# Optimization experiments

Measured on AMD Instinct MI355X. Metric: run time of the kernel, lower is better.

Reference implementation:

```python
import jax, jax.numpy as jnp
import numpy as np

D = 768
B = 32
N = 768


def setup_inputs() -> dict:
    key = jax.random.key(0)
    k1, k2, k3, k4 = jax.random.split(key, 4)
    stdv = 1.0 / np.sqrt(D)
    X = jax.random.normal(k1, (B, N, D), dtype=jnp.float32)
    adj = jax.random.uniform(k2, (B, N, N), dtype=jnp.float32)
    W_l = jax.random.uniform(k3, (D, D), dtype=jnp.float32, minval=-stdv, maxval=stdv)
    W_l1 = jax.random.uniform(k4, (D, D), dtype=jnp.float32, minval=-stdv, maxval=stdv)
    return {"X": X, "adj": adj, "W_l": W_l, "W_l1": W_l1}


def _row_normalize(adj):
    # rowsum^-1 with inf -> 0 (rows summing to zero stay zero)
    rowsum = adj.sum(axis=-1, keepdims=True)  # [B, N, 1]
    r_inv = jnp.where(rowsum == 0, 0.0, 1.0 / rowsum)
    return adj * r_inv


def reference(X, adj, W_l, W_l1):
    # X: [B, N, D], adj: [B, N, N]
    adj_n = _row_normalize(adj)
    e1 = jnp.einsum('bnd,de->bne', X, W_l1)        # message transform
    e11 = jnp.einsum('bnm,bmd->bnd', adj_n, e1)    # aggregate
    X1 = jnp.einsum('bnd,de->bne', X, W_l)         # self transform
    h = X1 + e11
    return jax.nn.leaky_relu(h, negative_slope=0.01)
```

## Files before the change

### kernel.cpp

```cpp
#include <hip/hip_runtime.h>
#include <hip/hip_bf16.h>
#include <cstdint>
#include <cstddef>

#define BN_ROWS 24576
#define DD 768
#define BE (768*768)
#define BM 192
#define BN_T 192
#define BK 32
#define ABUF 12288
#define BUFSZ 24576

typedef __attribute__((ext_vector_type(8))) short bf16x8;
typedef __attribute__((ext_vector_type(4))) float f32x4;
typedef __attribute__((ext_vector_type(8))) unsigned short u16x8;

static __device__ __forceinline__ unsigned short f2bf(float f) {
  unsigned int u = __builtin_bit_cast(unsigned int, f);
  unsigned int lsb = (u >> 16) & 1u;
  u += 0x7fffu + lsb;
  return (unsigned short)(u >> 16);
}

static __device__ __forceinline__ unsigned short f2bfv(float f) {
  __hip_bfloat16 h = __float2bfloat16(f);
  return __builtin_bit_cast(unsigned short, h);
}

static __device__ __forceinline__ bf16x8 cvt8(float4 u, float4 w, float sc) {
  bf16x8 o;
  o[0] = (short)f2bfv(u.x * sc); o[1] = (short)f2bfv(u.y * sc);
  o[2] = (short)f2bfv(u.z * sc); o[3] = (short)f2bfv(u.w * sc);
  o[4] = (short)f2bfv(w.x * sc); o[5] = (short)f2bfv(w.y * sc);
  o[6] = (short)f2bfv(w.z * sc); o[7] = (short)f2bfv(w.w * sc);
  return o;
}


#define P_AN 3072
#define P_WT 144
#define P_FL 288

__global__ __launch_bounds__(256) void prep(const float* __restrict__ adj,
                                            const float* __restrict__ Wl,
                                            const float* __restrict__ Wl1,
                                            unsigned short* __restrict__ adjnb,
                                            unsigned short* __restrict__ WlT,
                                            unsigned short* __restrict__ Wl1T) {
  __shared__ float tile[64][65];
  const int bid = blockIdx.x;
  if (bid < P_AN) {
    const int w = threadIdx.x >> 6;
    const int hl = (threadIdx.x >> 5) & 1;
    const int l = threadIdx.x & 31;
    const int row = bid * 8 + w * 2 + hl;
    const float4* a = reinterpret_cast<const float4*>(adj + (size_t)row * DD);
    float4 v[6];
    #pragma unroll
    for (int i = 0; i < 3; ++i) {
      int u = l + i * 32;
      v[2 * i]     = a[u * 2];
      v[2 * i + 1] = a[u * 2 + 1];
    }
    float s = 0.f;
    #pragma unroll
    for (int i = 0; i < 6; ++i) s += (v[i].x + v[i].y) + (v[i].z + v[i].w);
    #pragma unroll
    for (int off = 16; off; off >>= 1) s += __shfl_xor(s, off);
    float rinv = (s == 0.f) ? 0.f : 1.f / s;
    u16x8* o = reinterpret_cast<u16x8*>(adjnb + (size_t)row * DD);
    #pragma unroll
    for (int i = 0; i < 3; ++i)
      o[l + i * 32] = __builtin_bit_cast(u16x8, cvt8(v[2 * i], v[2 * i + 1], rinv));
  } else if (bid < P_AN + P_WT) {
    const int tb = bid - P_AN;
    const int tr = tb / 12, tc = tb % 12;
    const int c = threadIdx.x & 63, r0 = threadIdx.x >> 6;
    #pragma unroll
    for (int i = 0; i < 16; ++i) {
      int r = r0 + i * 4;
      tile[r][c] = Wl1[(size_t)(tr * 64 + r) * DD + tc * 64 + c];
    }
    __syncthreads();
    #pragma unroll
    for (int i = 0; i < 16; ++i) {
      int r2 = r0 + i * 4;
      Wl1T[(size_t)(tc * 64 + r2) * DD + tr * 64 + c] = f2bf(tile[c][r2]);
    }
  } else {
    const int b2 = bid - (P_AN + P_WT);
    const int wg = b2 * 4 + (threadIdx.x >> 6);
    const int lane = threadIdx.x & 63;
    const int d0 = (wg % 96) * 8;
    const int e = (wg / 96) * 64 + lane;
    u16x8 o;
    #pragma unroll
    for (int j = 0; j < 8; ++j)
      o[j] = f2bf(Wl[(size_t)(d0 + j) * DD + e]);
    const int base = ((e >> 4) * 24 + (d0 >> 5)) * 512
                   + ((e & 15) + (((d0 >> 3) & 3) << 4)) * 8;
    *reinterpret_cast<u16x8*>(WlT + base) = o;
  }
}

__global__ __launch_bounds__(256, 2) void gemm_e1(
    const float* __restrict__ X,
    const unsigned short* __restrict__ W1T,
    unsigned short* __restrict__ e1T,
    unsigned short* __restrict__ Xb)
{
  __shared__ char smem[2 * BUFSZ];
  constexpr int NT = 24;
  const int tid = threadIdx.x, lane = tid & 63;
  const int wid = tid >> 6;
  const int wr = wid >> 1, wc = wid & 1;

  const int logical = (blockIdx.x & 7) * 64 + (blockIdx.x >> 3);
  const int mt = logical >> 2, nt = logical & 3;
  const int b = mt >> 2;
  const float* Ag = X + (size_t)mt * BM * DD;
  const unsigned short* Bg = W1T + (size_t)nt * BN_T * DD;

  const int r_in = lane >> 2;
  const int s_in = lane & 3;

  float4 aR[3][2];
  auto issueA = [&](int s) {
    int kk = s < NT ? s : 0;
    #pragma unroll
    for (int i = 0; i < 3; ++i) {
      int row = (wid * 3 + i) * 16 + r_in;
      int slot = s_in ^ ((row >> 1) & 3);
      const float4* p = reinterpret_cast<const float4*>(
          Ag + (size_t)row * DD + kk * BK + slot * 8);
      aR[i][0] = p[0];
      aR[i][1] = p[1];
    }
  };
  auto writeA = [&](int s) {
    const int buf = (s & 1) * BUFSZ;
    #pragma unroll
    for (int i = 0; i < 3; ++i)
      *reinterpret_cast<bf16x8*>(smem + buf + (wid * 3 + i) * 1024 + lane * 16) =
          cvt8(aR[i][0], aR[i][1], 1.0f);
  };
  auto storeXb = [&](int s) {
    int kk = s < NT ? s : 0;
    #pragma unroll
    for (int i = 0; i < 3; ++i) {
      int row = (wid * 3 + i) * 16 + r_in;
      int slot = s_in ^ ((row >> 1) & 3);
      *reinterpret_cast<bf16x8*>(Xb + (size_t)(mt * BM + row) * DD + kk * BK + slot * 8) =
          cvt8(aR[i][0], aR[i][1], 1.0f);
    }
  };
  auto issueB = [&](int s) {
    int kk = s < NT ? s : 0;
    const int buf = (s & 1) * BUFSZ + ABUF;
    #pragma unroll
    for (int i = 0; i < 3; ++i) {
      int c = wid * 3 + i;
      int row = c * 16 + r_in;
      int slot = s_in ^ ((row >> 1) & 3);
      const unsigned short* src = Bg + (size_t)row * DD + kk * BK + slot * 8;
      __builtin_amdgcn_global_load_lds(
          (const __attribute__((address_space(1))) void*)src,
          (__attribute__((address_space(3))) void*)(smem + buf + c * 1024),
          16, 0, 0);
    }
  };

  const int ks = lane >> 4;
  auto frag = [&](int off, int row) -> bf16x8 {
    int slot = ks ^ ((row >> 1) & 3);
    return *reinterpret_cast<const bf16x8*>(smem + off + row * 64 + slot * 16);
  };

  f32x4 acc[6][6] = {};
  const int arow = wr * 96 + (lane & 15);
  const int brow = wc * 96 + (lane & 15);

  issueA(0);
  asm volatile("s_waitcnt vmcnt(0)" ::: "memory");
  writeA(0);
  issueB(0);
  issueA(1);
  asm volatile("s_waitcnt lgkmcnt(0)" ::: "memory");
  __builtin_amdgcn_s_barrier();

  for (int t = 0; t < NT; ++t) {
    asm volatile("s_waitcnt vmcnt(6)" ::: "memory");
    __builtin_amdgcn_s_barrier();
    issueB(t + 1);

    const int bufA = (t & 1) * BUFSZ;
    const int bufB = bufA + ABUF;
    bf16x8 a[6], bg[6];
    #pragma unroll
    for (int i = 0; i < 6; ++i) a[i] = frag(bufA, arow + i * 16);
    #pragma unroll
    for (int i = 0; i < 6; ++i) bg[i] = frag(bufB, brow + i * 16);

    __builtin_amdgcn_s_setprio(1);
    #pragma unroll
    for (int ni = 0; ni < 6; ++ni)
      #pragma unroll
      for (int mi = 0; mi < 6; ++mi)
        acc[mi][ni] = __builtin_amdgcn_mfma_f32_16x16x32_bf16(a[mi], bg[ni], acc[mi][ni], 0, 0, 0);
    __builtin_amdgcn_s_setprio(0);

    asm volatile("s_waitcnt vmcnt(3)" ::: "memory");
    writeA(t + 1);
    if (nt == 0) storeXb(t + 1);
    issueA(t + 2);
    asm volatile("s_waitcnt lgkmcnt(0)" ::: "memory");
  }

  unsigned short* ob = e1T + (size_t)b * BE;
  const int m0 = (mt & 3) * BM + wr * 96 + (lane >> 4) * 4;
  const int l15 = lane & 15;
  #pragma unroll
  for (int mi = 0; mi < 6; ++mi)
    #pragma unroll
    for (int ni = 0; ni < 6; ++ni) {
      int m = m0 + mi * 16;
      int cb = nt * 12 + wc * 6 + ni;
      int fa = (cb * 24 + (m >> 5)) * 512
             + (l15 + (((m >> 3) & 3) << 4)) * 8 + (m & 7);
      f32x4 v = acc[mi][ni];
      ushort4 o;
      o.x = f2bf(v[0]); o.y = f2bf(v[1]); o.z = f2bf(v[2]); o.w = f2bf(v[3]);
      *reinterpret_cast<ushort4*>(ob + fa) = o;
    }
}

__global__ __launch_bounds__(256, 2) void gemm_bg(
    const unsigned short* __restrict__ adjnb,
    const unsigned short* __restrict__ e1T,
    const unsigned short* __restrict__ Xb,
    const unsigned short* __restrict__ WlT,
    float* __restrict__ out)
{
  __shared__ char smem[24576];
  constexpr int NT = 48;
  const int tid = threadIdx.x, lane = tid & 63;
  const int wid = tid >> 6;
  const int wr = wid >> 1, wc = wid & 1;

  const int logical = (blockIdx.x & 7) * 64 + (blockIdx.x >> 3);
  const int b = logical >> 4;
  const int r = logical & 15;
  const int mt = r >> 2, nt = r & 3;
  const size_t bo = (size_t)b * BE;
  const unsigned short* A0 = adjnb + bo + (size_t)mt * BM * DD;
  const unsigned short* A1 = Xb + bo + (size_t)mt * BM * DD;
  const unsigned short* B0 = e1T + bo;
  const unsigned short* B1 = WlT;

  const int r_in = lane >> 2;
  const int s_in = lane & 3;
  const int colblk0 = nt * 12 + wc * 6;

  auto stage = [&](int s) {
    int sc = s < NT ? s : 0;
    const unsigned short* base = (sc >= 24) ? A1 : A0;
    int kk = (sc >= 24) ? sc - 24 : sc;
    const int buf = (s & 1) * 12288;
    #pragma unroll
    for (int i = 0; i < 3; ++i) {
      int chunk = wid * 3 + i;
      int row = chunk * 16 + r_in;
      int slot = s_in ^ ((row >> 1) & 3);
      const unsigned short* src = base + (size_t)row * DD + kk * BK + slot * 8;
      __builtin_amdgcn_global_load_lds(
          (const __attribute__((address_space(1))) void*)src,
          (__attribute__((address_space(3))) void*)(smem + buf + chunk * 1024),
          16, 0, 0);
    }
  };

  auto loadB = [&](int s, bf16x8* dst) {
    int sc = s < NT ? s : 0;
    const unsigned short* base = (sc >= 24) ? B1 : B0;
    int kk = (sc >= 24) ? sc - 24 : sc;
    #pragma unroll
    for (int ni = 0; ni < 6; ++ni)
      dst[ni] = *reinterpret_cast<const bf16x8*>(
          base + ((colblk0 + ni) * 24 + kk) * 512 + lane * 8);
  };

  const int ks = lane >> 4;
  auto rdA = [&](int off, int row) -> bf16x8 {
    int slot = ks ^ ((row >> 1) & 3);
    return *reinterpret_cast<const bf16x8*>(smem + off + row * 64 + slot * 16);
  };

  f32x4 acc[6][6] = {};
  const int arow = wr * 96 + (lane & 15);
  bf16x8 bA[6], bB[6];

  auto body = [&](int bufo, bf16x8* bfr) {
    #pragma unroll
    for (int mh = 0; mh < 2; ++mh) {
      bf16x8 a[3];
      #pragma unroll
      for (int i = 0; i < 3; ++i) a[i] = rdA(bufo, arow + mh * 48 + i * 16);
      __builtin_amdgcn_s_setprio(1);
      #pragma unroll
      for (int mi = 0; mi < 3; ++mi)
        #pragma unroll
        for (int ni = 0; ni < 6; ++ni)
          acc[mh * 3 + mi][ni] = __builtin_amdgcn_mfma_f32_16x16x32_bf16(
              a[mi], bfr[ni], acc[mh * 3 + mi][ni], 0, 0, 0);
      __builtin_amdgcn_s_setprio(0);
    }
  };

  stage(0); loadB(0, bA);
  for (int t = 0; t < NT; t += 2) {
    asm volatile("s_waitcnt vmcnt(6)" ::: "memory");
    __builtin_amdgcn_s_barrier();
    stage(t + 1); loadB(t + 1, bB);
    body(0, bA);
    asm volatile("s_waitcnt vmcnt(6)" ::: "memory");
    __builtin_amdgcn_s_barrier();
    stage(t + 2); loadB(t + 2, bA);
    body(12288, bB);
  }
  asm volatile("s_waitcnt vmcnt(0)" ::: "memory");

  float* ob = out + bo;
  const int m0 = mt * BM + wr * 96 + (lane >> 4) * 4;
  const int l15 = lane & 15;
  #pragma unroll
  for (int mi = 0; mi < 6; ++mi)
    #pragma unroll
    for (int ni = 0; ni < 6; ++ni) {
      int m = m0 + mi * 16;
      int n = nt * BN_T + wc * 96 + ni * 16 + l15;
      f32x4 v = acc[mi][ni];
      #pragma unroll
      for (int j = 0; j < 4; ++j) {
        float x = v[j];
        ob[(size_t)(m + j) * DD + n] = x > 0.f ? x : 0.01f * x;
      }
    }
}


extern "C" void kernel_launch(void* const* d_in, const int* in_sizes, int n_in,
                              void* d_out, int out_size, void* d_ws, size_t ws_size,
                              hipStream_t stream) {
  const float* X   = (const float*)d_in[0];
  const float* adj = (const float*)d_in[1];
  const float* Wl  = (const float*)d_in[2];
  const float* Wl1 = (const float*)d_in[3];
  float* out = (float*)d_out;

  char* ws = (char*)d_ws;
  const size_t SZ = (size_t)BN_ROWS * DD * 2;
  unsigned short* e1T   = (unsigned short*)(ws);
  unsigned short* adjnb = (unsigned short*)(ws + SZ);
  unsigned short* Xb    = (unsigned short*)(ws + 2 * SZ);
  unsigned short* WlT   = (unsigned short*)(ws + 3 * SZ);
  unsigned short* Wl1T  = (unsigned short*)(ws + 3 * SZ + (size_t)BE * 2);

  prep<<<P_AN + P_WT + P_FL, 256, 0, stream>>>(adj, Wl, Wl1, adjnb, WlT, Wl1T);
  gemm_e1<<<512, 256, 0, stream>>>(X, Wl1T, e1T, Xb);
  gemm_bg<<<512, 256, 0, stream>>>(adjnb, e1T, Xb, WlT, out);
}
```

Baseline: 157.9 us.

## Compute X·W_l in first GEMM kernel and add it in the aggregate epilogue

After: 154.1 us. 2.4% less time.

```diff
diff --git a/kernel.cpp b/kernel.cpp
--- a/kernel.cpp
+++ b/kernel.cpp
@@ -7,10 +7,7 @@
 #define DD 768
 #define BE (768*768)
 #define BM 192
-#define BN_T 192
 #define BK 32
-#define ABUF 12288
-#define BUFSZ 24576
 
 typedef __attribute__((ext_vector_type(8))) short bf16x8;
 typedef __attribute__((ext_vector_type(4))) float f32x4;
@@ -22,24 +19,29 @@
   u += 0x7fffu + lsb;
   return (unsigned short)(u >> 16);
 }
-
 static __device__ __forceinline__ unsigned short f2bfv(float f) {
   __hip_bfloat16 h = __float2bfloat16(f);
   return __builtin_bit_cast(unsigned short, h);
 }
-
-static __device__ __forceinline__ bf16x8 cvt8(float4 u, float4 w, float sc) {
+static __device__ __forceinline__ bf16x8 cvt8(float4 u, float4 w) {
   bf16x8 o;
-  o[0] = (short)f2bfv(u.x * sc); o[1] = (short)f2bfv(u.y * sc);
-  o[2] = (short)f2bfv(u.z * sc); o[3] = (short)f2bfv(u.w * sc);
-  o[4] = (short)f2bfv(w.x * sc); o[5] = (short)f2bfv(w.y * sc);
-  o[6] = (short)f2bfv(w.z * sc); o[7] = (short)f2bfv(w.w * sc);
+  o[0] = (short)f2bfv(u.x); o[1] = (short)f2bfv(u.y);
+  o[2] = (short)f2bfv(u.z); o[3] = (short)f2bfv(u.w);
+  o[4] = (short)f2bfv(w.x); o[5] = (short)f2bfv(w.y);
+  o[6] = (short)f2bfv(w.z); o[7] = (short)f2bfv(w.w);
   return o;
 }
+static __device__ __forceinline__ u16x8 pack8s(float4 a, float4 b, float sc) {
+  u16x8 o;
+  o[0] = f2bfv(a.x * sc); o[1] = f2bfv(a.y * sc);
+  o[2] = f2bfv(a.z * sc); o[3] = f2bfv(a.w * sc);
+  o[4] = f2bfv(b.x * sc); o[5] = f2bfv(b.y * sc);
+  o[6] = f2bfv(b.z * sc); o[7] = f2bfv(b.w * sc);
+  return o;
+}
 
 
 #define P_AN 3072
-#define P_WT 144
 #define P_FL 288
 
 __global__ __launch_bounds__(256) void prep(const float* __restrict__ adj,
@@ -48,7 +50,6 @@
                                             unsigned short* __restrict__ adjnb,
                                             unsigned short* __restrict__ WlT,
                                             unsigned short* __restrict__ Wl1T) {
-  __shared__ float tile[64][65];
   const int bid = blockIdx.x;
   if (bid < P_AN) {
     const int w = threadIdx.x >> 6;
@@ -72,55 +73,46 @@
     u16x8* o = reinterpret_cast<u16x8*>(adjnb + (size_t)row * DD);
     #pragma unroll
     for (int i = 0; i < 3; ++i)
-      o[l + i * 32] = __builtin_bit_cast(u16x8, cvt8(v[2 * i], v[2 * i + 1], rinv));
-  } else if (bid < P_AN + P_WT) {
-    const int tb = bid - P_AN;
-    const int tr = tb / 12, tc = tb % 12;
-    const int c = threadIdx.x & 63, r0 = threadIdx.x >> 6;
-    #pragma unroll
-    for (int i = 0; i < 16; ++i) {
-      int r = r0 + i * 4;
-      tile[r][c] = Wl1[(size_t)(tr * 64 + r) * DD + tc * 64 + c];
-    }
-    __syncthreads();
-    #pragma unroll
-    for (int i = 0; i < 16; ++i) {
-      int r2 = r0 + i * 4;
-      Wl1T[(size_t)(tc * 64 + r2) * DD + tr * 64 + c] = f2bf(tile[c][r2]);
-    }
+      o[l + i * 32] = pack8s(v[2 * i], v[2 * i + 1], rinv);
   } else {
-    const int b2 = bid - (P_AN + P_WT);
-    const int wg = b2 * 4 + (threadIdx.x >> 6);
+    const int b2 = bid - P_AN;
+    const bool isWl = b2 < P_FL;
+    const int b3 = isWl ? b2 : b2 - P_FL;
+    const float* src = isWl ? Wl : Wl1;
+    unsigned short* dst = isWl ? WlT : Wl1T;
+    const int wg = b3 * 4 + (threadIdx.x >> 6);
     const int lane = threadIdx.x & 63;
     const int d0 = (wg % 96) * 8;
     const int e = (wg / 96) * 64 + lane;
     u16x8 o;
     #pragma unroll
     for (int j = 0; j < 8; ++j)
-      o[j] = f2bf(Wl[(size_t)(d0 + j) * DD + e]);
+      o[j] = f2bf(src[(size_t)(d0 + j) * DD + e]);
     const int base = ((e >> 4) * 24 + (d0 >> 5)) * 512
                    + ((e & 15) + (((d0 >> 3) & 3) << 4)) * 8;
-    *reinterpret_cast<u16x8*>(WlT + base) = o;
+    *reinterpret_cast<u16x8*>(dst + base) = o;
   }
 }
 
-__global__ __launch_bounds__(256, 2) void gemm_e1(
+__global__ __launch_bounds__(256, 2) void e1w(
     const float* __restrict__ X,
-    const unsigned short* __restrict__ W1T,
+    const unsigned short* __restrict__ Wl1T,
+    const unsigned short* __restrict__ WlT,
     unsigned short* __restrict__ e1T,
-    unsigned short* __restrict__ Xb)
+    unsigned short* __restrict__ X1f)
 {
-  __shared__ char smem[2 * BUFSZ];
+  __shared__ char smem[2 * 12288];
   constexpr int NT = 24;
   const int tid = threadIdx.x, lane = tid & 63;
   const int wid = tid >> 6;
   const int wr = wid >> 1, wc = wid & 1;
 
-  const int logical = (blockIdx.x & 7) * 64 + (blockIdx.x >> 3);
-  const int mt = logical >> 2, nt = logical & 3;
+  const int logical = (blockIdx.x & 7) * 128 + (blockIdx.x >> 3);
+  const int mt = logical >> 3, nt = logical & 7;
   const int b = mt >> 2;
   const float* Ag = X + (size_t)mt * BM * DD;
-  const unsigned short* Bg = W1T + (size_t)nt * BN_T * DD;
+  const unsigned short* Bfl = (nt < 4) ? Wl1T : WlT;
+  const int colblk0 = (nt & 3) * 12 + wc * 6;
 
   const int r_in = lane >> 2;
   const int s_in = lane & 3;
@@ -139,111 +131,114 @@
     }
   };
   auto writeA = [&](int s) {
-    const int buf = (s & 1) * BUFSZ;
+    const int buf = (s & 1) * 12288;
     #pragma unroll
     for (int i = 0; i < 3; ++i)
       *reinterpret_cast<bf16x8*>(smem + buf + (wid * 3 + i) * 1024 + lane * 16) =
-          cvt8(aR[i][0], aR[i][1], 1.0f);
-  };
-  auto storeXb = [&](int s) {
+          cvt8(aR[i][0], aR[i][1]);
+  };
+  auto loadB = [&](int s, bf16x8* dst) {
     int kk = s < NT ? s : 0;
     #pragma unroll
-    for (int i = 0; i < 3; ++i) {
-      int row = (wid * 3 + i) * 16 + r_in;
-      int slot = s_in ^ ((row >> 1) & 3);
-      *reinterpret_cast<bf16x8*>(Xb + (size_t)(mt * BM + row) * DD + kk * BK + slot * 8) =
-          cvt8(aR[i][0], aR[i][1], 1.0f);
-    }
-  };
-  auto issueB = [&](int s) {
-    int kk = s < NT ? s : 0;
-    const int buf = (s & 1) * BUFSZ + ABUF;
-    #pragma unroll
-    for (int i = 0; i < 3; ++i) {
-      int c = wid * 3 + i;
-      int row = c * 16 + r_in;
-      int slot = s_in ^ ((row >> 1) & 3);
-      const unsigned short* src = Bg + (size_t)row * DD + kk * BK + slot * 8;
-      __builtin_amdgcn_global_load_lds(
-          (const __attribute__((address_space(1))) void*)src,
-          (__attribute__((address_space(3))) void*)(smem + buf + c * 1024),
-          16, 0, 0);
-    }
+    for (int ni = 0; ni < 6; ++ni)
+      dst[ni] = *reinterpret_cast<const bf16x8*>(
+          Bfl + ((colblk0 + ni) * 24 + kk) * 512 + lane * 8);
   };
 
   const int ks = lane >> 4;
-  auto frag = [&](int off, int row) -> bf16x8 {
+  auto rdA = [&](int off, int row) -> bf16x8 {
     int slot = ks ^ ((row >> 1) & 3);
     return *reinterpret_cast<const bf16x8*>(smem + off + row * 64 + slot * 16);
   };
 
   f32x4 acc[6][6] = {};
   const int arow = wr * 96 + (lane & 15);
-  const int brow = wc * 96 + (lane & 15);
+  bf16x8 bA[6], bB[6];
+
+  auto body = [&](int bufo, bf16x8* bfr) {
+    #pragma unroll
+    for (int mh = 0; mh < 2; ++mh) {
+      bf16x8 a[3];
+      #pragma unroll
+      for (int i = 0; i < 3; ++i) a[i] = rdA(bufo, arow + mh * 48 + i * 16);
+      __builtin_amdgcn_s_setprio(1);
+      #pragma unroll
+      for (int mi = 0; mi < 3; ++mi)
+        #pragma unroll
+        for (int ni = 0; ni < 6; ++ni)
+          acc[mh * 3 + mi][ni] = __builtin_amdgcn_mfma_f32_16x16x32_bf16(
+              a[mi], bfr[ni], acc[mh * 3 + mi][ni], 0, 0, 0);
+      __builtin_amdgcn_s_setprio(0);
+    }
+  };
 
   issueA(0);
   asm volatile("s_waitcnt vmcnt(0)" ::: "memory");
   writeA(0);
-  issueB(0);
+  loadB(0, bA);
   issueA(1);
   asm volatile("s_waitcnt lgkmcnt(0)" ::: "memory");
   __builtin_amdgcn_s_barrier();
 
-  for (int t = 0; t < NT; ++t) {
+  for (int t = 0; t < NT; t += 2) {
+    loadB(t + 1, bB);
+    body(0, bA);
     asm volatile("s_waitcnt vmcnt(6)" ::: "memory");
-    __builtin_amdgcn_s_barrier();
-    issueB(t + 1);
-
-    const int bufA = (t & 1) * BUFSZ;
-    const int bufB = bufA + ABUF;
-    bf16x8 a[6], bg[6];
-    #pragma unroll
-    for (int i = 0; i < 6; ++i) a[i] = frag(bufA, arow + i * 16);
-    #pragma unroll
-    for (int i = 0; i < 6; ++i) bg[i] = frag(bufB, brow + i * 16);
-
-    __builtin_amdgcn_s_setprio(1);
-    #pragma unroll
-    for (int ni = 0; ni < 6; ++ni)
-      #pragma unroll
-      for (int mi = 0; mi < 6; ++mi)
-        acc[mi][ni] = __builtin_amdgcn_mfma_f32_16x16x32_bf16(a[mi], bg[ni], acc[mi][ni], 0, 0, 0);
-    __builtin_amdgcn_s_setprio(0);
-
-    asm volatile("s_waitcnt vmcnt(3)" ::: "memory");
     writeA(t + 1);
-    if (nt == 0) storeXb(t + 1);
     issueA(t + 2);
     asm volatile("s_waitcnt lgkmcnt(0)" ::: "memory");
+    __builtin_amdgcn_s_barrier();
+
+    loadB(t + 2, bA);
+    body(12288, bB);
+    asm volatile("s_waitcnt vmcnt(6)" ::: "memory");
+    writeA(t + 2);
+    issueA(t + 3);
+    asm volatile("s_waitcnt lgkmcnt(0)" ::: "memory");
+    __builtin_amdgcn_s_barrier();
   }
-
-  unsigned short* ob = e1T + (size_t)b * BE;
-  const int m0 = (mt & 3) * BM + wr * 96 + (lane >> 4) * 4;
+  asm volatile("s_waitcnt vmcnt(0)" ::: "memory");
+
   const int l15 = lane & 15;
-  #pragma unroll
-  for (int mi = 0; mi < 6; ++mi)
-    #pragma unroll
-    for (int ni = 0; ni < 6; ++ni) {
-      int m = m0 + mi * 16;
-      int cb = nt * 12 + wc * 6 + ni;
-      int fa = (cb * 24 + (m >> 5)) * 512
-             + (l15 + (((m >> 3) & 3) << 4)) * 8 + (m & 7);
-      f32x4 v = acc[mi][ni];
-      ushort4 o;
-      o.x = f2bf(v[0]); o.y = f2bf(v[1]); o.z = f2bf(v[2]); o.w = f2bf(v[3]);
-      *reinterpret_cast<ushort4*>(ob + fa) = o;
-    }
+  if (nt < 4) {
+    unsigned short* ob = e1T + (size_t)b * BE;
+    const int m0 = (mt & 3) * BM + wr * 96 + (lane >> 4) * 4;
+    #pragma unroll
+    for (int mi = 0; mi < 6; ++mi)
+      #pragma unroll
+      for (int ni = 0; ni < 6; ++ni) {
+        int m = m0 + mi * 16;
+        int cb = nt * 12 + wc * 6 + ni;
+        int fa = (cb * 24 + (m >> 5)) * 512
+               + (l15 + (((m >> 3) & 3) << 4)) * 8 + (m & 7);
+        f32x4 v = acc[mi][ni];
+        ushort4 o;
+        o.x = f2bf(v[0]); o.y = f2bf(v[1]); o.z = f2bf(v[2]); o.w = f2bf(v[3]);
+        *reinterpret_cast<ushort4*>(ob + fa) = o;
+      }
+  } else {
+    const int flat = b * 16 + (mt & 3) * 4 + (nt - 4);
+    ushort4* o4 = reinterpret_cast<ushort4*>(X1f) + (size_t)flat * 36 * 256 + tid;
+    #pragma unroll
+    for (int mi = 0; mi < 6; ++mi)
+      #pragma unroll
+      for (int ni = 0; ni < 6; ++ni) {
+        f32x4 v = acc[mi][ni];
+        ushort4 o;
+        o.x = f2bf(v[0]); o.y = f2bf(v[1]); o.z = f2bf(v[2]); o.w = f2bf(v[3]);
+        o4[(mi * 6 + ni) * 256] = o;
+      }
+  }
 }
 
 __global__ __launch_bounds__(256, 2) void gemm_bg(
     const unsigned short* __restrict__ adjnb,
     const unsigned short* __restrict__ e1T,
-    const unsigned short* __restrict__ Xb,
-    const unsigned short* __restrict__ WlT,
+    const unsigned short* __restrict__ X1f,
     float* __restrict__ out)
 {
   __shared__ char smem[24576];
-  constexpr int NT = 48;
+  constexpr int NT = 24;
   const int tid = threadIdx.x, lane = tid & 63;
   const int wid = tid >> 6;
   const int wr = wid >> 1, wc = wid & 1;
@@ -254,40 +249,33 @@
   const int mt = r >> 2, nt = r & 3;
   const size_t bo = (size_t)b * BE;
   const unsigned short* A0 = adjnb + bo + (size_t)mt * BM * DD;
-  const unsigned short* A1 = Xb + bo + (size_t)mt * BM * DD;
   const unsigned short* B0 = e1T + bo;
-  const unsigned short* B1 = WlT;
 
   const int r_in = lane >> 2;
   const int s_in = lane & 3;
   const int colblk0 = nt * 12 + wc * 6;
 
   auto stage = [&](int s) {
-    int sc = s < NT ? s : 0;
-    const unsigned short* base = (sc >= 24) ? A1 : A0;
-    int kk = (sc >= 24) ? sc - 24 : sc;
+    int kk = s < NT ? s : 0;
     const int buf = (s & 1) * 12288;
     #pragma unroll
     for (int i = 0; i < 3; ++i) {
       int chunk = wid * 3 + i;
       int row = chunk * 16 + r_in;
       int slot = s_in ^ ((row >> 1) & 3);
-      const unsigned short* src = base + (size_t)row * DD + kk * BK + slot * 8;
+      const unsigned short* src = A0 + (size_t)row * DD + kk * BK + slot * 8;
       __builtin_amdgcn_global_load_lds(
           (const __attribute__((address_space(1))) void*)src,
           (__attribute__((address_space(3))) void*)(smem + buf + chunk * 1024),
           16, 0, 0);
     }
   };
-
   auto loadB = [&](int s, bf16x8* dst) {
-    int sc = s < NT ? s : 0;
-    const unsigned short* base = (sc >= 24) ? B1 : B0;
-    int kk = (sc >= 24) ? sc - 24 : sc;
+    int kk = s < NT ? s : 0;
     #pragma unroll
     for (int ni = 0; ni < 6; ++ni)
       dst[ni] = *reinterpret_cast<const bf16x8*>(
-          base + ((colblk0 + ni) * 24 + kk) * 512 + lane * 8);
+          B0 + ((colblk0 + ni) * 24 + kk) * 512 + lane * 8);
   };
 
   const int ks = lane >> 4;
@@ -333,16 +321,24 @@
   float* ob = out + bo;
   const int m0 = mt * BM + wr * 96 + (lane >> 4) * 4;
   const int l15 = lane & 15;
+  const int flat = b * 16 + mt * 4 + nt;
+  const ushort4* x4 = reinterpret_cast<const ushort4*>(X1f) + (size_t)flat * 36 * 256 + tid;
   #pragma unroll
   for (int mi = 0; mi < 6; ++mi)
     #pragma unroll
     for (int ni = 0; ni < 6; ++ni) {
       int m = m0 + mi * 16;
-      int n = nt * BN_T + wc * 96 + ni * 16 + l15;
+      int n = nt * 192 + wc * 96 + ni * 16 + l15;
+      ushort4 xi = x4[(mi * 6 + ni) * 256];
       f32x4 v = acc[mi][ni];
+      float x1v[4];
+      x1v[0] = __builtin_bit_cast(float, (unsigned int)xi.x << 16);
+      x1v[1] = __builtin_bit_cast(float, (unsigned int)xi.y << 16);
+      x1v[2] = __builtin_bit_cast(float, (unsigned int)xi.z << 16);
+      x1v[3] = __builtin_bit_cast(float, (unsigned int)xi.w << 16);
       #pragma unroll
       for (int j = 0; j < 4; ++j) {
-        float x = v[j];
+        float x = v[j] + x1v[j];
         ob[(size_t)(m + j) * DD + n] = x > 0.f ? x : 0.01f * x;
       }
     }
@@ -362,11 +358,11 @@
   const size_t SZ = (size_t)BN_ROWS * DD * 2;
   unsigned short* e1T   = (unsigned short*)(ws);
   unsigned short* adjnb = (unsigned short*)(ws + SZ);
-  unsigned short* Xb    = (unsigned short*)(ws + 2 * SZ);
+  unsigned short* X1f   = (unsigned short*)(ws + 2 * SZ);
   unsigned short* WlT   = (unsigned short*)(ws + 3 * SZ);
   unsigned short* Wl1T  = (unsigned short*)(ws + 3 * SZ + (size_t)BE * 2);
 
-  prep<<<P_AN + P_WT + P_FL, 256, 0, stream>>>(adj, Wl, Wl1, adjnb, WlT, Wl1T);
-  gemm_e1<<<512, 256, 0, stream>>>(X, Wl1T, e1T, Xb);
-  gemm_bg<<<512, 256, 0, stream>>>(adjnb, e1T, Xb, WlT, out);
-}
+  prep<<<P_AN + 2 * P_FL, 256, 0, stream>>>(adj, Wl, Wl1, adjnb, WlT, Wl1T);
+  e1w<<<1024, 256, 0, stream>>>(X, Wl1T, WlT, e1T, X1f);
+  gemm_bg<<<512, 256, 0, stream>>>(adjnb, e1T, X1f, out);
+}
```
